# Performance work log

Measured on AMD Instinct MI355X. Metric: run time of the kernel, lower is better.

The kernel has to match this reference:

```python
import jax, jax.numpy as jnp
import numpy as np

B, V, S, H, I, L, NH = 32, 50, 64, 256, 512, 2, 4
VOCAB, SEGV, AGEV = 30000, 2, 144
EPS = 1e-12


def _ln(x, g, b):
    m = jnp.mean(x, axis=-1, keepdims=True)
    v = jnp.mean((x - m) ** 2, axis=-1, keepdims=True)
    return (x - m) / jnp.sqrt(v + EPS) * g + b


def _sinusoid_table(max_pos, hidden):
    pos = np.arange(max_pos, dtype=np.float32)[:, None]
    idx = np.arange(hidden, dtype=np.float32)[None, :]
    ang = pos / np.power(10000.0, 2.0 * idx / hidden)
    tab = np.where((np.arange(hidden) % 2 == 0)[None, :], np.sin(ang), np.cos(ang))
    return jnp.asarray(tab, dtype=jnp.float32)


def setup_inputs() -> dict:
    key = jax.random.key(0)
    ks = iter(jax.random.split(key, 48))

    def nrm(shape, s=0.02):
        return jax.random.normal(next(ks), shape, dtype=jnp.float32) * s

    inp = {
        "word": jax.random.randint(next(ks), (B, V, S), 0, VOCAB),
        "age": jax.random.randint(next(ks), (B, V, S), 0, AGEV),
        "seg": jax.random.randint(next(ks), (B, V, S), 0, SEGV),
        "posi": jax.random.randint(next(ks), (B, V, S), 0, S),
        "mask": jnp.ones((B, V, S), dtype=jnp.float32),
        "token": 0,
        "word_emb": nrm((VOCAB, H)),
        "seg_emb": nrm((SEGV, H)),
        "age_emb": nrm((AGEV, H)),
        "posi_emb": _sinusoid_table(S, H),
        "emb_ln_g": jnp.ones((H,), jnp.float32),
        "emb_ln_b": jnp.zeros((H,), jnp.float32),
        "qw": nrm((L, H, H)), "qb": jnp.zeros((L, H), jnp.float32),
        "kw": nrm((L, H, H)), "kb": jnp.zeros((L, H), jnp.float32),
        "vw": nrm((L, H, H)), "vb": jnp.zeros((L, H), jnp.float32),
        "ow": nrm((L, H, H)), "ob": jnp.zeros((L, H), jnp.float32),
        "attn_ln_g": jnp.ones((L, H), jnp.float32),
        "attn_ln_b": jnp.zeros((L, H), jnp.float32),
        "iw": nrm((L, H, I)), "ib": jnp.zeros((L, I), jnp.float32),
        "outw": nrm((L, I, H)), "outb": jnp.zeros((L, H), jnp.float32),
        "out_ln_g": jnp.ones((L, H), jnp.float32),
        "out_ln_b": jnp.zeros((L, H), jnp.float32),
        "pool_w": nrm((H, H)), "pool_b": jnp.zeros((H,), jnp.float32),
    }
    return inp


def reference(word, age, seg, posi, mask, token,
              word_emb, seg_emb, age_emb, posi_emb, emb_ln_g, emb_ln_b,
              qw, qb, kw, kb, vw, vb, ow, ob, attn_ln_g, attn_ln_b,
              iw, ib, outw, outb, out_ln_g, out_ln_b, pool_w, pool_b):
    # token embeddings: word + seg + age + sinusoidal position, then LayerNorm
    emb = word_emb[word] + seg_emb[seg] + age_emb[age] + posi_emb[posi]  # [B,V,S,H]
    x = _ln(emb, emb_ln_g, emb_ln_b)
    N = B * V
    x = x.reshape(N, S, H)  # vectorize the per-visit loop over the batch axis
    am = ((1.0 - mask) * -10000.0).reshape(N, 1, 1, S)  # additive attention mask
    d = H // NH
    scale = 1.0 / jnp.sqrt(jnp.float32(d))
    n_layers = qw.shape[0]
    for l in range(n_layers):
        q = (x @ qw[l] + qb[l]).reshape(N, S, NH, d)
        k = (x @ kw[l] + kb[l]).reshape(N, S, NH, d)
        v = (x @ vw[l] + vb[l]).reshape(N, S, NH, d)
        scores = jnp.einsum("bqhd,bkhd->bhqk", q, k) * scale + am
        probs = jax.nn.softmax(scores, axis=-1)  # dropout = identity (eval)
        ctx = jnp.einsum("bhqk,bkhd->bqhd", probs, v).reshape(N, S, H)
        a = _ln(ctx @ ow[l] + ob[l] + x, attn_ln_g[l], attn_ln_b[l])
        h = jax.nn.gelu(a @ iw[l] + ib[l], approximate=False)
        x = _ln(h @ outw[l] + outb[l] + a, out_ln_g[l], out_ln_b[l])
    first = x[:, 0].reshape(B, V, H)  # pooler with token=False: hidden[:, 0]
    return jnp.tanh(first @ pool_w + pool_b)  # [B, V, H]
```

## Files before the change

kernel.cpp:

```cpp
#include <hip/hip_runtime.h>
#include <math.h>

typedef __attribute__((ext_vector_type(8))) short short8;
typedef __attribute__((ext_vector_type(4))) short short4v;
typedef __attribute__((ext_vector_type(4))) float f32x4;

#define M_TOT 102400

__device__ __forceinline__ unsigned short f2b(float f) {
  unsigned u = __float_as_uint(f);
  return (unsigned short)((u + 0x7fffu + ((u >> 16) & 1u)) >> 16);
}
__device__ __forceinline__ float b2f(unsigned short h) {
  return __uint_as_float(((unsigned)h) << 16);
}
__device__ __forceinline__ f32x4 mfma16(short8 a, short8 b, f32x4 c) {
  return __builtin_amdgcn_mfma_f32_16x16x32_bf16(a, b, c, 0, 0, 0);
}
template <int STRIDE>
__device__ __forceinline__ short8 lds8(const short* buf, int row, int k) {
  int idx = (row * STRIDE + k) ^ ((row & 7) << 3);
  return *(const short8*)(buf + idx);
}
template <int STRIDE>
__device__ __forceinline__ void ldsw(short* buf, int row, int col, unsigned short v) {
  buf[(row * STRIDE + col) ^ ((row & 7) << 3)] = (short)v;
}
__device__ __forceinline__ float red16sum(float v) {
  v += __shfl_xor(v, 1); v += __shfl_xor(v, 2);
  v += __shfl_xor(v, 4); v += __shfl_xor(v, 8);
  return v;
}
__device__ __forceinline__ float red16max(float v) {
  v = fmaxf(v, __shfl_xor(v, 1)); v = fmaxf(v, __shfl_xor(v, 2));
  v = fmaxf(v, __shfl_xor(v, 4)); v = fmaxf(v, __shfl_xor(v, 8));
  return v;
}

__device__ __forceinline__ void stage16k(const short* __restrict__ g, short* l,
                                         int w, int lane) {
  const char* gb = (const char*)g + w * 4096 + lane * 16;
  char* lb = (char*)l + w * 4096;
#pragma unroll
  for (int c = 0; c < 4; ++c)
    __builtin_amdgcn_global_load_lds(
        (const __attribute__((address_space(1))) unsigned int*)(gb + c * 1024),
        (__attribute__((address_space(3))) unsigned int*)(lb + c * 1024), 16, 0, 0);
}

template <int KB>
__device__ __forceinline__ void gemm_core(const short* __restrict__ A, int lda,
                                          const short* __restrict__ Wimg,
                                          short* sB, f32x4 acc[16], int r0,
                                          int w, int lane, int l15, int g4) {
  short8 af[KB];
#pragma unroll
  for (int kk = 0; kk < KB; ++kk)
    af[kk] = *(const short8*)(A + (r0 + l15) * lda + kk * 32 + g4 * 8);
  stage16k(Wimg, sB, w, lane);
  __syncthreads();
#pragma unroll
  for (int kb = 0; kb < KB; ++kb) {
    if (kb + 1 < KB)
      stage16k(Wimg + (kb + 1) * 8192, sB + ((kb + 1) & 1) * 8192, w, lane);
    const short* cur = sB + (kb & 1) * 8192;
#pragma unroll
    for (int tc = 0; tc < 16; ++tc) {
      int row = tc * 16 + l15;
      short8 bf = *(const short8*)(cur + ((row * 32 + g4 * 8) ^ ((row & 7) << 3)));
      acc[tc] = mfma16(af[kb], bf, acc[tc]);
    }
    __syncthreads();
  }
}

__device__ __forceinline__ void ln_epi(f32x4 acc[16], short* x,
                                       const float* __restrict__ bias,
                                       const float* __restrict__ g_,
                                       const float* __restrict__ b_,
                                       int r0, int l15, int g4) {
  float s1[4] = {0.f, 0.f, 0.f, 0.f}, s2[4] = {0.f, 0.f, 0.f, 0.f};
#pragma unroll
  for (int tc = 0; tc < 16; ++tc) {
    int col = tc * 16 + l15;
    float bv = bias[col];
#pragma unroll
    for (int r = 0; r < 4; ++r) {
      float v = acc[tc][r] + bv + b2f((unsigned short)x[(r0 + g4 * 4 + r) * 256 + col]);
      acc[tc][r] = v;
      s1[r] += v; s2[r] += v * v;
    }
  }
  float mean[4], rstd[4];
#pragma unroll
  for (int r = 0; r < 4; ++r) {
    float a = red16sum(s1[r]), q = red16sum(s2[r]);
    mean[r] = a * (1.f / 256.f);
    rstd[r] = rsqrtf(q * (1.f / 256.f) - mean[r] * mean[r] + 1e-12f);
  }
#pragma unroll
  for (int tc = 0; tc < 16; ++tc) {
    int col = tc * 16 + l15;
    float gv = g_[col], bv = b_[col];
#pragma unroll
    for (int r = 0; r < 4; ++r)
      x[(r0 + g4 * 4 + r) * 256 + col] =
          (short)f2b((acc[tc][r] - mean[r]) * rstd[r] * gv + bv);
  }
}

__global__ void prep_w(const float* __restrict__ qw, const float* __restrict__ kw,
                       const float* __restrict__ vw, const float* __restrict__ ow,
                       const float* __restrict__ iw, const float* __restrict__ outw,
                       const float* __restrict__ pw, short* __restrict__ ws) {
  int t = blockIdx.x * 256 + threadIdx.x;
  float val; int base, n, k;
  if (t < 524288) {
    int which = t >> 17, r = t & 131071;
    int ly = r >> 16, e = r & 65535;
    n = e >> 8; k = e & 255;
    const float* m = which == 0 ? qw : which == 1 ? kw : which == 2 ? vw : ow;
    val = m[(ly * 256 + k) * 256 + n];
    base = which * 131072 + ly * 65536;
  } else if (t < 786432) {
    int e = t - 524288;
    int ly = e >> 17, f = e & 131071, g2 = f >> 16, e2 = f & 65535;
    n = e2 >> 8; k = e2 & 255;
    val = iw[(ly * 256 + k) * 512 + g2 * 256 + n];
    base = 524288 + ly * 131072 + g2 * 65536;
  } else if (t < 1048576) {
    int e = t - 786432;
    int ly = e >> 17, f = e & 131071;
    n = f >> 9; k = f & 511;
    val = outw[(ly * 512 + k) * 256 + n];
    base = 786432 + ly * 131072;
  } else {
    int e = t - 1048576;
    n = e >> 8; k = e & 255;
    val = pw[k * 256 + n];
    base = 1048576;
  }
  int pos = ((n * 32 + (k & 31)) ^ ((n & 7) << 3));
  ws[base + (k >> 5) * 8192 + pos] = (short)f2b(val);
}

__global__ __launch_bounds__(256) void emb_k(
    const int* __restrict__ word, const int* __restrict__ age,
    const int* __restrict__ seg, const int* __restrict__ posi,
    const float* __restrict__ we, const float* __restrict__ se,
    const float* __restrict__ ae, const float* __restrict__ pe,
    const float* __restrict__ g, const float* __restrict__ b,
    short* __restrict__ x) {
  int w = threadIdx.x >> 6, lane = threadIdx.x & 63;
  int t = blockIdx.x * 4 + w;
  int wi = word[t], gi = seg[t], ai = age[t], pi = posi[t];
  f32x4 e = ((const f32x4*)(we + wi * 256))[lane];
  f32x4 tv = ((const f32x4*)(se + gi * 256))[lane]; e = e + tv;
  tv = ((const f32x4*)(ae + ai * 256))[lane]; e = e + tv;
  tv = ((const f32x4*)(pe + pi * 256))[lane]; e = e + tv;
  float s1 = e[0] + e[1] + e[2] + e[3];
  float s2 = e[0] * e[0] + e[1] * e[1] + e[2] * e[2] + e[3] * e[3];
#pragma unroll
  for (int m = 1; m < 64; m <<= 1) { s1 += __shfl_xor(s1, m); s2 += __shfl_xor(s2, m); }
  float mean = s1 * (1.f / 256.f);
  float rstd = rsqrtf(s2 * (1.f / 256.f) - mean * mean + 1e-12f);
  f32x4 gv = ((const f32x4*)g)[lane];
  f32x4 bv = ((const f32x4*)b)[lane];
  short4v pk;
#pragma unroll
  for (int j = 0; j < 4; ++j) pk[j] = (short)f2b((e[j] - mean) * rstd * gv[j] + bv[j]);
  *(short4v*)(x + t * 256 + lane * 4) = pk;
}

__global__ __launch_bounds__(256) void qkv3_k(
    const short* __restrict__ x, const short* __restrict__ img,
    const float* __restrict__ qb_, const float* __restrict__ kb_,
    const float* __restrict__ vb_,
    short* __restrict__ q, short* __restrict__ k2, short* __restrict__ vt, int ly) {
  __shared__ __align__(16) short sB[16384];
  int w = threadIdx.x >> 6, lane = threadIdx.x & 63;
  int l15 = lane & 15, g4 = lane >> 4;
  int y = blockIdx.y;
  int r0 = blockIdx.x * 64 + w * 16;
  const short* W = img + y * 131072 + ly * 65536;
  const float* bias = (y == 0 ? qb_ : y == 1 ? kb_ : vb_) + ly * 256;
  f32x4 acc[16];
#pragma unroll
  for (int i = 0; i < 16; ++i) acc[i] = f32x4{0.f, 0.f, 0.f, 0.f};
  gemm_core<8>(x, 256, W, sB, acc, r0, w, lane, l15, g4);
  if (y < 2) {
    short* out = y ? k2 : q;
#pragma unroll
    for (int tc = 0; tc < 16; ++tc) {
      int col = tc * 16 + l15;
      float bv = bias[col];
#pragma unroll
      for (int r = 0; r < 4; ++r)
        out[(r0 + g4 * 4 + r) * 256 + col] = (short)f2b(acc[tc][r] + bv);
    }
  } else {
#pragma unroll
    for (int tc = 0; tc < 16; ++tc) {
      int col = tc * 16 + l15;
      float bv = bias[col];
#pragma unroll
      for (int r = 0; r < 4; ++r) {
        int tok = r0 + g4 * 4 + r;
        vt[(tok >> 6) * 16384 + col * 64 + (tok & 63)] = (short)f2b(acc[tc][r] + bv);
      }
    }
  }
}

__global__ __launch_bounds__(256) void attn_k(
    const short* __restrict__ q, const short* __restrict__ k,
    const short* __restrict__ vt, short* __restrict__ ctx,
    const float* __restrict__ mask) {
  __shared__ __align__(16) short sP[16384];
  int w = threadIdx.x >> 6, lane = threadIdx.x & 63;
  int l15 = lane & 15, g4 = lane >> 4;
  int n = blockIdx.x;
  const f32x4 zero4 = {0.f, 0.f, 0.f, 0.f};
  short* sPw = sP + w * 4096;

  float amvr[4];
#pragma unroll
  for (int tc = 0; tc < 4; ++tc)
    amvr[tc] = (1.f - mask[n * 64 + tc * 16 + l15]) * -10000.f;

  const short* qn = q + n * 16384;
  const short* kn = k + n * 16384;
  const short* vtn = vt + n * 16384;

  short8 qa[4][2];
#pragma unroll
  for (int st = 0; st < 4; ++st)
#pragma unroll
    for (int ks = 0; ks < 2; ++ks)
      qa[st][ks] = *(const short8*)(qn + (st * 16 + l15) * 256 + w * 64 + ks * 32 + g4 * 8);
  f32x4 sacc[4][4];
#pragma unroll
  for (int st = 0; st < 4; ++st)
#pragma unroll
    for (int tc = 0; tc < 4; ++tc) sacc[st][tc] = zero4;
#pragma unroll
  for (int ks = 0; ks < 2; ++ks)
#pragma unroll
    for (int tc = 0; tc < 4; ++tc) {
      short8 kf = *(const short8*)(kn + (tc * 16 + l15) * 256 + w * 64 + ks * 32 + g4 * 8);
#pragma unroll
      for (int st = 0; st < 4; ++st) sacc[st][tc] = mfma16(qa[st][ks], kf, sacc[st][tc]);
    }
#pragma unroll
  for (int st = 0; st < 4; ++st)
#pragma unroll
    for (int r = 0; r < 4; ++r) {
      float pv[4];
      float mx = -1e30f;
#pragma unroll
      for (int tc = 0; tc < 4; ++tc) {
        float sv = sacc[st][tc][r] * 0.125f + amvr[tc];
        pv[tc] = sv;
        mx = fmaxf(mx, sv);
      }
      mx = red16max(mx);
      float sm = 0.f;
#pragma unroll
      for (int tc = 0; tc < 4; ++tc) {
        float e = __expf(pv[tc] - mx);
        pv[tc] = e;
        sm += e;
      }
      sm = red16sum(sm);
      float inv = 1.f / sm;
#pragma unroll
      for (int tc = 0; tc < 4; ++tc)
        ldsw<64>(sPw, st * 16 + g4 * 4 + r, tc * 16 + l15, f2b(pv[tc] * inv));
    }
  __syncthreads();

  f32x4 cacc[4][4];
#pragma unroll
  for (int st = 0; st < 4; ++st)
#pragma unroll
    for (int tc = 0; tc < 4; ++tc) cacc[st][tc] = zero4;
#pragma unroll
  for (int ks = 0; ks < 2; ++ks) {
    short8 pa[4];
#pragma unroll
    for (int st = 0; st < 4; ++st) pa[st] = lds8<64>(sPw, st * 16 + l15, ks * 32 + g4 * 8);
#pragma unroll
    for (int tc = 0; tc < 4; ++tc) {
      short8 vf = *(const short8*)(vtn + (w * 64 + tc * 16 + l15) * 64 + ks * 32 + g4 * 8);
#pragma unroll
      for (int st = 0; st < 4; ++st) cacc[st][tc] = mfma16(pa[st], vf, cacc[st][tc]);
    }
  }
#pragma unroll
  for (int st = 0; st < 4; ++st)
#pragma unroll
    for (int tc = 0; tc < 4; ++tc)
#pragma unroll
      for (int r = 0; r < 4; ++r)
        ctx[(n * 64 + st * 16 + g4 * 4 + r) * 256 + w * 64 + tc * 16 + l15] =
            (short)f2b(cacc[st][tc][r]);
}

__global__ __launch_bounds__(256) void oln_k(
    const short* __restrict__ ctx, const short* __restrict__ img,
    const float* __restrict__ bias, short* __restrict__ x,
    const float* __restrict__ g_, const float* __restrict__ b_) {
  __shared__ __align__(16) short sB[16384];
  int w = threadIdx.x >> 6, lane = threadIdx.x & 63;
  int l15 = lane & 15, g4 = lane >> 4;
  int r0 = blockIdx.x * 64 + w * 16;
  f32x4 acc[16];
#pragma unroll
  for (int i = 0; i < 16; ++i) acc[i] = f32x4{0.f, 0.f, 0.f, 0.f};
  gemm_core<8>(ctx, 256, img, sB, acc, r0, w, lane, l15, g4);
  ln_epi(acc, x, bias, g_, b_, r0, l15, g4);
}

__global__ __launch_bounds__(256) void ffn1_k(
    const short* __restrict__ x, const short* __restrict__ img,
    const float* __restrict__ bias, short* __restrict__ h) {
  __shared__ __align__(16) short sB[16384];
  int w = threadIdx.x >> 6, lane = threadIdx.x & 63;
  int l15 = lane & 15, g4 = lane >> 4;
  int y = blockIdx.y;
  int r0 = blockIdx.x * 64 + w * 16;
  f32x4 acc[16];
#pragma unroll
  for (int i = 0; i < 16; ++i) acc[i] = f32x4{0.f, 0.f, 0.f, 0.f};
  gemm_core<8>(x, 256, img + y * 65536, sB, acc, r0, w, lane, l15, g4);
  const float* bs = bias + y * 256;
#pragma unroll
  for (int tc = 0; tc < 16; ++tc) {
    int col = tc * 16 + l15;
    float bv = bs[col];
#pragma unroll
    for (int r = 0; r < 4; ++r) {
      float v = acc[tc][r] + bv;
      v = 0.5f * v * (1.f + erff(v * 0.70710678118f));
      h[(r0 + g4 * 4 + r) * 512 + y * 256 + col] = (short)f2b(v);
    }
  }
}

__global__ __launch_bounds__(256) void ffn2_k(
    const short* __restrict__ h, const short* __restrict__ img,
    const float* __restrict__ bias, short* __restrict__ x,
    const float* __restrict__ g_, const float* __restrict__ b_) {
  __shared__ __align__(16) short sB[16384];
  int w = threadIdx.x >> 6, lane = threadIdx.x & 63;
  int l15 = lane & 15, g4 = lane >> 4;
  int r0 = blockIdx.x * 64 + w * 16;
  f32x4 acc[16];
#pragma unroll
  for (int i = 0; i < 16; ++i) acc[i] = f32x4{0.f, 0.f, 0.f, 0.f};
  gemm_core<16>(h, 512, img, sB, acc, r0, w, lane, l15, g4);
  ln_epi(acc, x, bias, g_, b_, r0, l15, g4);
}

__global__ __launch_bounds__(256) void pool_k(
    const short* __restrict__ x, const short* __restrict__ img,
    const float* __restrict__ pb, float* __restrict__ out) {
  __shared__ __align__(16) short sB[16384];
  int w = threadIdx.x >> 6, lane = threadIdx.x & 63;
  int l15 = lane & 15, g4 = lane >> 4;
  int r0 = blockIdx.x * 64 + w * 16;
  f32x4 acc[16];
#pragma unroll
  for (int i = 0; i < 16; ++i) acc[i] = f32x4{0.f, 0.f, 0.f, 0.f};
  gemm_core<8>(x, 16384, img, sB, acc, r0, w, lane, l15, g4);
#pragma unroll
  for (int tc = 0; tc < 16; ++tc) {
    int col = tc * 16 + l15;
    float bv = pb[col];
#pragma unroll
    for (int r = 0; r < 4; ++r)
      out[(r0 + g4 * 4 + r) * 256 + col] = tanhf(acc[tc][r] + bv);
  }
}

extern "C" void kernel_launch(void* const* d_in, const int* in_sizes, int n_in,
                              void* d_out, int out_size, void* d_ws, size_t ws_size,
                              hipStream_t stream) {
  const int* word = (const int*)d_in[0];
  const int* age = (const int*)d_in[1];
  const int* seg = (const int*)d_in[2];
  const int* posi = (const int*)d_in[3];
  const float* mask = (const float*)d_in[4];
  const float* word_emb = (const float*)d_in[6];
  const float* seg_emb = (const float*)d_in[7];
  const float* age_emb = (const float*)d_in[8];
  const float* posi_emb = (const float*)d_in[9];
  const float* emb_g = (const float*)d_in[10];
  const float* emb_b = (const float*)d_in[11];
  const float* qw = (const float*)d_in[12];
  const float* qb = (const float*)d_in[13];
  const float* kw = (const float*)d_in[14];
  const float* kb = (const float*)d_in[15];
  const float* vw = (const float*)d_in[16];
  const float* vb = (const float*)d_in[17];
  const float* ow = (const float*)d_in[18];
  const float* ob = (const float*)d_in[19];
  const float* attn_g = (const float*)d_in[20];
  const float* attn_b = (const float*)d_in[21];
  const float* iw = (const float*)d_in[22];
  const float* ib = (const float*)d_in[23];
  const float* outw = (const float*)d_in[24];
  const float* outb = (const float*)d_in[25];
  const float* out_g = (const float*)d_in[26];
  const float* out_b = (const float*)d_in[27];
  const float* pool_w = (const float*)d_in[28];
  const float* pool_b = (const float*)d_in[29];
  short* ws = (short*)d_ws;

  short* xb_ = ws + 1114112;
  short* qbuf = xb_ + 26214400;
  short* kbuf = qbuf + 26214400;
  short* vtbuf = kbuf + 26214400;
  short* hbuf = qbuf;

  prep_w<<<4352, 256, 0, stream>>>(qw, kw, vw, ow, iw, outw, pool_w, ws);
  emb_k<<<25600, 256, 0, stream>>>(word, age, seg, posi, word_emb, seg_emb,
                                   age_emb, posi_emb, emb_g, emb_b, xb_);
  for (int ly = 0; ly < 2; ++ly) {
    qkv3_k<<<dim3(1600, 3), 256, 0, stream>>>(xb_, ws, qb, kb, vb, qbuf, kbuf,
                                              vtbuf, ly);
    attn_k<<<1600, 256, 0, stream>>>(qbuf, kbuf, vtbuf, qbuf, mask);
    oln_k<<<1600, 256, 0, stream>>>(qbuf, ws + 393216 + ly * 65536, ob + ly * 256,
                                    xb_, attn_g + ly * 256, attn_b + ly * 256);
    ffn1_k<<<dim3(1600, 2), 256, 0, stream>>>(xb_, ws + 524288 + ly * 131072,
                                              ib + ly * 512, hbuf);
    ffn2_k<<<1600, 256, 0, stream>>>(hbuf, ws + 786432 + ly * 131072,
                                     outb + ly * 256, xb_, out_g + ly * 256,
                                     out_b + ly * 256);
  }
  pool_k<<<25, 256, 0, stream>>>(xb_, ws + 1048576, pool_b, (float*)d_out);
}
```

Measured before the change: 709.3 us.

## Stage GEMM and attention epilogue outputs through LDS for coalesced 16-byte stores

Epilogues in qkv, attention, ffn1, oln and ffn2 kernels used to write scattered 2-byte bf16 values straight to global memory, including a strided transposed store for V. They now write the tile into swizzled shared memory, synchronize, and copy it out as contiguous 16-byte vectors. The residual read in the LayerNorm epilogue is also loaded into LDS with coalesced vector loads. This adds extra barriers and LDS traffic, and reuses the GEMM staging buffer, in exchange for far fewer, wider global memory transactions.

```diff
diff --git a/kernel.cpp b/kernel.cpp
--- a/kernel.cpp
+++ b/kernel.cpp
@@ -4,8 +4,6 @@
 typedef __attribute__((ext_vector_type(8))) short short8;
 typedef __attribute__((ext_vector_type(4))) short short4v;
 typedef __attribute__((ext_vector_type(4))) float f32x4;
-
-#define M_TOT 102400
 
 __device__ __forceinline__ unsigned short f2b(float f) {
   unsigned u = __float_as_uint(f);
@@ -74,11 +72,21 @@
   }
 }
 
-__device__ __forceinline__ void ln_epi(f32x4 acc[16], short* x,
-                                       const float* __restrict__ bias,
-                                       const float* __restrict__ g_,
-                                       const float* __restrict__ b_,
-                                       int r0, int l15, int g4) {
+__device__ __forceinline__ void ln_epi2(f32x4 acc[16], short* __restrict__ x,
+                                        short* sB,
+                                        const float* __restrict__ bias,
+                                        const float* __restrict__ g_,
+                                        const float* __restrict__ b_,
+                                        int r0b, int w, int tid, int l15, int g4) {
+  const short* xsrc = x + (size_t)r0b * 256;
+#pragma unroll
+  for (int i = 0; i < 8; ++i) {
+    int j = i * 256 + tid;
+    int row = j >> 5, c8 = j & 31;
+    short8 v = *(const short8*)(xsrc + j * 8);
+    *(short8*)(sB + ((row * 256 + c8 * 8) ^ ((row & 7) << 3))) = v;
+  }
+  __syncthreads();
   float s1[4] = {0.f, 0.f, 0.f, 0.f}, s2[4] = {0.f, 0.f, 0.f, 0.f};
 #pragma unroll
   for (int tc = 0; tc < 16; ++tc) {
@@ -86,7 +94,9 @@
     float bv = bias[col];
 #pragma unroll
     for (int r = 0; r < 4; ++r) {
-      float v = acc[tc][r] + bv + b2f((unsigned short)x[(r0 + g4 * 4 + r) * 256 + col]);
+      int lrow = w * 16 + g4 * 4 + r;
+      float v = acc[tc][r] + bv +
+                b2f((unsigned short)sB[(lrow * 256 + col) ^ ((lrow & 7) << 3)]);
       acc[tc][r] = v;
       s1[r] += v; s2[r] += v * v;
     }
@@ -94,18 +104,29 @@
   float mean[4], rstd[4];
 #pragma unroll
   for (int r = 0; r < 4; ++r) {
-    float a = red16sum(s1[r]), q = red16sum(s2[r]);
+    float a = red16sum(s1[r]), qq = red16sum(s2[r]);
     mean[r] = a * (1.f / 256.f);
-    rstd[r] = rsqrtf(q * (1.f / 256.f) - mean[r] * mean[r] + 1e-12f);
+    rstd[r] = rsqrtf(qq * (1.f / 256.f) - mean[r] * mean[r] + 1e-12f);
   }
 #pragma unroll
   for (int tc = 0; tc < 16; ++tc) {
     int col = tc * 16 + l15;
     float gv = g_[col], bv = b_[col];
 #pragma unroll
-    for (int r = 0; r < 4; ++r)
-      x[(r0 + g4 * 4 + r) * 256 + col] =
+    for (int r = 0; r < 4; ++r) {
+      int lrow = w * 16 + g4 * 4 + r;
+      sB[(lrow * 256 + col) ^ ((lrow & 7) << 3)] =
           (short)f2b((acc[tc][r] - mean[r]) * rstd[r] * gv + bv);
+    }
+  }
+  __syncthreads();
+  short* xdst = x + (size_t)r0b * 256;
+#pragma unroll
+  for (int i = 0; i < 8; ++i) {
+    int j = i * 256 + tid;
+    int row = j >> 5, c8 = j & 31;
+    short8 v = *(const short8*)(sB + ((row * 256 + c8 * 8) ^ ((row & 7) << 3)));
+    *(short8*)(xdst + j * 8) = v;
   }
 }
 
@@ -178,10 +199,12 @@
     const float* __restrict__ vb_,
     short* __restrict__ q, short* __restrict__ k2, short* __restrict__ vt, int ly) {
   __shared__ __align__(16) short sB[16384];
-  int w = threadIdx.x >> 6, lane = threadIdx.x & 63;
+  int tid = threadIdx.x;
+  int w = tid >> 6, lane = tid & 63;
   int l15 = lane & 15, g4 = lane >> 4;
   int y = blockIdx.y;
-  int r0 = blockIdx.x * 64 + w * 16;
+  int n = blockIdx.x;
+  int r0 = n * 64 + w * 16;
   const short* W = img + y * 131072 + ly * 65536;
   const float* bias = (y == 0 ? qb_ : y == 1 ? kb_ : vb_) + ly * 256;
   f32x4 acc[16];
@@ -189,14 +212,15 @@
   for (int i = 0; i < 16; ++i) acc[i] = f32x4{0.f, 0.f, 0.f, 0.f};
   gemm_core<8>(x, 256, W, sB, acc, r0, w, lane, l15, g4);
   if (y < 2) {
-    short* out = y ? k2 : q;
 #pragma unroll
     for (int tc = 0; tc < 16; ++tc) {
       int col = tc * 16 + l15;
       float bv = bias[col];
 #pragma unroll
-      for (int r = 0; r < 4; ++r)
-        out[(r0 + g4 * 4 + r) * 256 + col] = (short)f2b(acc[tc][r] + bv);
+      for (int r = 0; r < 4; ++r) {
+        int lrow = w * 16 + g4 * 4 + r;
+        sB[(lrow * 256 + col) ^ ((lrow & 7) << 3)] = (short)f2b(acc[tc][r] + bv);
+      }
     }
   } else {
 #pragma unroll
@@ -205,10 +229,26 @@
       float bv = bias[col];
 #pragma unroll
       for (int r = 0; r < 4; ++r) {
-        int tok = r0 + g4 * 4 + r;
-        vt[(tok >> 6) * 16384 + col * 64 + (tok & 63)] = (short)f2b(acc[tc][r] + bv);
+        int lrow = w * 16 + g4 * 4 + r;
+        sB[(col * 64 + lrow) ^ ((col & 7) << 3)] = (short)f2b(acc[tc][r] + bv);
       }
     }
+  }
+  __syncthreads();
+  short* dst = (y == 0 ? q : y == 1 ? k2 : vt) + (size_t)n * 16384;
+#pragma unroll
+  for (int i = 0; i < 8; ++i) {
+    int j = i * 256 + tid;
+    int idx;
+    if (y < 2) {
+      int row = j >> 5, c8 = j & 31;
+      idx = (row * 256 + c8 * 8) ^ ((row & 7) << 3);
+    } else {
+      int col = j >> 3, rb = j & 7;
+      idx = (col * 64 + rb * 8) ^ ((col & 7) << 3);
+    }
+    short8 v = *(const short8*)(sB + idx);
+    *(short8*)(dst + j * 8) = v;
   }
 }
 
@@ -216,21 +256,22 @@
     const short* __restrict__ q, const short* __restrict__ k,
     const short* __restrict__ vt, short* __restrict__ ctx,
     const float* __restrict__ mask) {
-  __shared__ __align__(16) short sP[16384];
-  int w = threadIdx.x >> 6, lane = threadIdx.x & 63;
+  __shared__ __align__(16) short sAll[16384];
+  int tid = threadIdx.x;
+  int w = tid >> 6, lane = tid & 63;
   int l15 = lane & 15, g4 = lane >> 4;
   int n = blockIdx.x;
   const f32x4 zero4 = {0.f, 0.f, 0.f, 0.f};
-  short* sPw = sP + w * 4096;
+  short* sPw = sAll + w * 4096;
 
   float amvr[4];
 #pragma unroll
   for (int tc = 0; tc < 4; ++tc)
     amvr[tc] = (1.f - mask[n * 64 + tc * 16 + l15]) * -10000.f;
 
-  const short* qn = q + n * 16384;
-  const short* kn = k + n * 16384;
-  const short* vtn = vt + n * 16384;
+  const short* qn = q + (size_t)n * 16384;
+  const short* kn = k + (size_t)n * 16384;
+  const short* vtn = vt + (size_t)n * 16384;
 
   short8 qa[4][2];
 #pragma unroll
@@ -296,14 +337,26 @@
       for (int st = 0; st < 4; ++st) cacc[st][tc] = mfma16(pa[st], vf, cacc[st][tc]);
     }
   }
+  __syncthreads();
 #pragma unroll
   for (int st = 0; st < 4; ++st)
 #pragma unroll
     for (int tc = 0; tc < 4; ++tc)
 #pragma unroll
-      for (int r = 0; r < 4; ++r)
-        ctx[(n * 64 + st * 16 + g4 * 4 + r) * 256 + w * 64 + tc * 16 + l15] =
-            (short)f2b(cacc[st][tc][r]);
+      for (int r = 0; r < 4; ++r) {
+        int lrow = st * 16 + g4 * 4 + r;
+        int col = w * 64 + tc * 16 + l15;
+        sAll[(lrow * 256 + col) ^ ((lrow & 7) << 3)] = (short)f2b(cacc[st][tc][r]);
+      }
+  __syncthreads();
+  short* dst = ctx + (size_t)n * 16384;
+#pragma unroll
+  for (int i = 0; i < 8; ++i) {
+    int j = i * 256 + tid;
+    int row = j >> 5, c8 = j & 31;
+    short8 v = *(const short8*)(sAll + ((row * 256 + c8 * 8) ^ ((row & 7) << 3)));
+    *(short8*)(dst + j * 8) = v;
+  }
 }
 
 __global__ __launch_bounds__(256) void oln_k(
@@ -311,28 +364,30 @@
     const float* __restrict__ bias, short* __restrict__ x,
     const float* __restrict__ g_, const float* __restrict__ b_) {
   __shared__ __align__(16) short sB[16384];
-  int w = threadIdx.x >> 6, lane = threadIdx.x & 63;
+  int tid = threadIdx.x;
+  int w = tid >> 6, lane = tid & 63;
   int l15 = lane & 15, g4 = lane >> 4;
-  int r0 = blockIdx.x * 64 + w * 16;
+  int r0b = blockIdx.x * 64;
   f32x4 acc[16];
 #pragma unroll
   for (int i = 0; i < 16; ++i) acc[i] = f32x4{0.f, 0.f, 0.f, 0.f};
-  gemm_core<8>(ctx, 256, img, sB, acc, r0, w, lane, l15, g4);
-  ln_epi(acc, x, bias, g_, b_, r0, l15, g4);
+  gemm_core<8>(ctx, 256, img, sB, acc, r0b + w * 16, w, lane, l15, g4);
+  ln_epi2(acc, x, sB, bias, g_, b_, r0b, w, tid, l15, g4);
 }
 
 __global__ __launch_bounds__(256) void ffn1_k(
     const short* __restrict__ x, const short* __restrict__ img,
     const float* __restrict__ bias, short* __restrict__ h) {
   __shared__ __align__(16) short sB[16384];
-  int w = threadIdx.x >> 6, lane = threadIdx.x & 63;
+  int tid = threadIdx.x;
+  int w = tid >> 6, lane = tid & 63;
   int l15 = lane & 15, g4 = lane >> 4;
   int y = blockIdx.y;
-  int r0 = blockIdx.x * 64 + w * 16;
+  int r0b = blockIdx.x * 64;
   f32x4 acc[16];
 #pragma unroll
   for (int i = 0; i < 16; ++i) acc[i] = f32x4{0.f, 0.f, 0.f, 0.f};
-  gemm_core<8>(x, 256, img + y * 65536, sB, acc, r0, w, lane, l15, g4);
+  gemm_core<8>(x, 256, img + y * 65536, sB, acc, r0b + w * 16, w, lane, l15, g4);
   const float* bs = bias + y * 256;
 #pragma unroll
   for (int tc = 0; tc < 16; ++tc) {
@@ -342,8 +397,18 @@
     for (int r = 0; r < 4; ++r) {
       float v = acc[tc][r] + bv;
       v = 0.5f * v * (1.f + erff(v * 0.70710678118f));
-      h[(r0 + g4 * 4 + r) * 512 + y * 256 + col] = (short)f2b(v);
-    }
+      int lrow = w * 16 + g4 * 4 + r;
+      sB[(lrow * 256 + col) ^ ((lrow & 7) << 3)] = (short)f2b(v);
+    }
+  }
+  __syncthreads();
+  short* dst = h + (size_t)r0b * 512 + y * 256;
+#pragma unroll
+  for (int i = 0; i < 8; ++i) {
+    int j = i * 256 + tid;
+    int row = j >> 5, c8 = j & 31;
+    short8 v = *(const short8*)(sB + ((row * 256 + c8 * 8) ^ ((row & 7) << 3)));
+    *(short8*)(dst + row * 512 + c8 * 8) = v;
   }
 }
 
@@ -352,14 +417,15 @@
     const float* __restrict__ bias, short* __restrict__ x,
     const float* __restrict__ g_, const float* __restrict__ b_) {
   __shared__ __align__(16) short sB[16384];
-  int w = threadIdx.x >> 6, lane = threadIdx.x & 63;
+  int tid = threadIdx.x;
+  int w = tid >> 6, lane = tid & 63;
   int l15 = lane & 15, g4 = lane >> 4;
-  int r0 = blockIdx.x * 64 + w * 16;
+  int r0b = blockIdx.x * 64;
   f32x4 acc[16];
 #pragma unroll
   for (int i = 0; i < 16; ++i) acc[i] = f32x4{0.f, 0.f, 0.f, 0.f};
-  gemm_core<16>(h, 512, img, sB, acc, r0, w, lane, l15, g4);
-  ln_epi(acc, x, bias, g_, b_, r0, l15, g4);
+  gemm_core<16>(h, 512, img, sB, acc, r0b + w * 16, w, lane, l15, g4);
+  ln_epi2(acc, x, sB, bias, g_, b_, r0b, w, tid, l15, g4);
 }
 
 __global__ __launch_bounds__(256) void pool_k(
@@ -379,7 +445,7 @@
     float bv = pb[col];
 #pragma unroll
     for (int r = 0; r < 4; ++r)
-      out[(r0 + g4 * 4 + r) * 256 + col] = tanhf(acc[tc][r] + bv);
+      out[(size_t)(r0 + g4 * 4 + r) * 256 + col] = tanhf(acc[tc][r] + bv);
   }
 }
 
```

New measurement: 819.2 us. 15.5% more time.
